# Kernel tuning notes

Measured on AMD Instinct MI355X. Metric: run time of the kernel, lower is better.

## Reference

```python
import jax, jax.numpy as jnp
import numpy as np

DIM = 768
HEADS = 12
HEAD_DIM = DIM // HEADS  # 64
B, T = 4, 2048


def setup_inputs() -> dict:
    key = jax.random.key(0)
    k1, k2, k3 = jax.random.split(key, 3)
    x = jax.random.normal(k1, (B, T, DIM), dtype=jnp.float32)
    w_qkv = jax.random.normal(k2, (DIM, 3 * DIM), dtype=jnp.float32) * (DIM ** -0.5)
    w_out = jax.random.normal(k3, (DIM, DIM), dtype=jnp.float32) * (DIM ** -0.5)
    b_out = jnp.zeros((DIM,), dtype=jnp.float32)
    return {"x": x, "w_qkv": w_qkv, "w_out": w_out, "b_out": b_out}


def reference(x, w_qkv, w_out, b_out):
    b, t, _ = x.shape
    # fused QKV projection (no bias)
    xp = x @ w_qkv                               # (b, t, 3*dim)
    # faithful to einops 'b t (d k h) -> k b h t d' with k=3, h=HEADS
    xp = xp.reshape(b, t, HEAD_DIM, 3, HEADS)
    qkv = jnp.transpose(xp, (3, 0, 4, 1, 2))     # (3, b, h, t, d)
    q, k, v = qkv[0], qkv[1], qkv[2]
    scores = jnp.einsum('bhid,bhjd->bhij', q, k) * (HEAD_DIM ** -0.5)
    attn = jax.nn.softmax(scores, axis=-1)
    out = jnp.einsum('bhij,bhjd->bhid', attn, v)  # (b, h, t, d)
    out = jnp.transpose(out, (0, 2, 1, 3)).reshape(b, t, HEADS * HEAD_DIM)
    return out @ w_out + b_out
```

## Files before the change

kernel.cpp:

```cpp
#include <hip/hip_runtime.h>
#include <hip/hip_bf16.h>


typedef short short8 __attribute__((ext_vector_type(8)));
typedef _Float16 half8 __attribute__((ext_vector_type(8)));
typedef _Float16 half2v __attribute__((ext_vector_type(2)));
typedef float f32x16 __attribute__((ext_vector_type(16)));
typedef unsigned int uint4v __attribute__((ext_vector_type(4)));
typedef unsigned short ushort8v __attribute__((ext_vector_type(8)));
typedef unsigned short ushort4v __attribute__((ext_vector_type(4)));
typedef unsigned short ushort;

__device__ __forceinline__ ushort f2h(float x) {
    _Float16 h = (_Float16)x;
    return __builtin_bit_cast(ushort, h);
}
__device__ __forceinline__ float h2f(ushort u) {
    return (float)__builtin_bit_cast(_Float16, u);
}
__device__ __forceinline__ unsigned pk2h(float lo, float hi) {
    return __builtin_bit_cast(unsigned, __builtin_amdgcn_cvt_pkrtz(lo, hi));
}
__device__ __forceinline__ float dot2acc(unsigned pair, float acc) {
    const half2v ones = {(_Float16)1.0f, (_Float16)1.0f};
    return __builtin_amdgcn_fdot2(__builtin_bit_cast(half2v, pair), ones, acc, false);
}
__device__ __forceinline__ short8 ldfrag(const ushort* buf, int row, int slotLogical) {
    int phys = slotLogical ^ (row & 7);
    return *reinterpret_cast<const short8*>(&buf[row * 64 + phys * 8]);
}
__device__ __forceinline__ f32x16 mfma16(half8 a, half8 b, f32x16 c) {
    return __builtin_amdgcn_mfma_f32_32x32x16_f16(a, b, c, 0, 0, 0);
}
__device__ __forceinline__ half8 ldfragh(const ushort* buf, int row, int slotLogical) {
    return __builtin_bit_cast(half8, ldfrag(buf, row, slotLogical));
}
__device__ __forceinline__ half8 ldh(const ushort* p) {
    return __builtin_bit_cast(half8, *reinterpret_cast<const short8*>(p));
}
__device__ __forceinline__ void gload16(const ushort* g, ushort* l) {
    __builtin_amdgcn_global_load_lds((__attribute__((address_space(1))) void*)g,
                                     (__attribute__((address_space(3))) void*)l, 16, 0, 0);
}

__global__ __launch_bounds__(256) void prep_all(const float* __restrict__ x,
                                                const float* __restrict__ wqkv,
                                                const float* __restrict__ wout,
                                                ushort* __restrict__ Xh,
                                                ushort* __restrict__ Wt,
                                                ushort* __restrict__ Wo) {
    int b = blockIdx.x;
    if (b < 3072) {
        long i8 = (long)(b * 256 + threadIdx.x) * 8;
        float4 v0 = *reinterpret_cast<const float4*>(&x[i8]);
        float4 v1 = *reinterpret_cast<const float4*>(&x[i8 + 4]);
        float v[8] = {v0.x, v0.y, v0.z, v0.w, v1.x, v1.y, v1.z, v1.w};
        ushort8v hh;
#pragma unroll
        for (int j = 0; j < 8; ++j) hh[j] = f2h(v[j]);
        *reinterpret_cast<ushort8v*>(&Xh[i8]) = hh;
    } else if (b < 3072 + 864) {
        int id = (b - 3072) * 256 + threadIdx.x;
        int n = id % 2304;
        int oct = id / 2304;
        int g = n >> 6, d = n & 63;
        int col = d * 36 + g;
        ushort8v hh;
#pragma unroll
        for (int i = 0; i < 8; ++i) hh[i] = f2h(wqkv[(long)(8 * oct + i) * 2304 + col]);
        *reinterpret_cast<ushort8v*>(&Wt[(long)n * 768 + 8 * oct]) = hh;
    } else {
        int id = (b - 3936) * 256 + threadIdx.x;
        int n = id % 768;
        int oct = id / 768;
        ushort8v hh;
#pragma unroll
        for (int i = 0; i < 8; ++i) hh[i] = f2h(wout[(long)(8 * oct + i) * 768 + n]);
        *reinterpret_cast<ushort8v*>(&Wo[(long)n * 768 + 8 * oct]) = hh;
    }
}

__device__ __forceinline__ void gemm_core(const ushort* __restrict__ A,
                                          const ushort* __restrict__ Bt,
                                          long aBase, long bBase,
                                          ushort* sA, ushort* sB, f32x16 (&acc)[2][2]) {
    const int tid = threadIdx.x;
    const int lane = tid & 63, w = tid >> 6;
    const int c31 = lane & 31, g1 = lane >> 5;
    const int wr = w >> 1, wc = w & 1;
    const int srow_in_chunk = lane >> 3;
    for (int k0 = 0; k0 < 768; k0 += 64) {
        __syncthreads();
#pragma unroll
        for (int t = 0; t < 4; ++t) {
            int row = w * 32 + t * 8 + srow_in_chunk;
            int sl = (lane & 7) ^ (row & 7);
            long goff = (long)row * 768 + k0 + sl * 8;
            int ldst = (w * 32 + t * 8) * 64;
            gload16(&A[aBase + goff], &sA[ldst]);
            gload16(&Bt[bBase + goff], &sB[ldst]);
        }
        __syncthreads();
#pragma unroll
        for (int ks = 0; ks < 4; ++ks) {
            half8 ah[2], bh[2];
#pragma unroll
            for (int i = 0; i < 2; ++i) {
                ah[i] = ldfragh(sA, wr * 64 + i * 32 + c31, 2 * ks + g1);
                bh[i] = ldfragh(sB, wc * 64 + i * 32 + c31, 2 * ks + g1);
            }
#pragma unroll
            for (int mi = 0; mi < 2; ++mi)
#pragma unroll
                for (int nj = 0; nj < 2; ++nj)
                    acc[mi][nj] = mfma16(ah[mi], bh[nj], acc[mi][nj]);
        }
    }
}

__global__ __launch_bounds__(256) void gemm_qkv(const ushort* __restrict__ Xh,
                                                const ushort* __restrict__ Wt,
                                                ushort* __restrict__ Qf,
                                                ushort* __restrict__ Kf,
                                                ushort* __restrict__ Vt) {
    __shared__ ushort sA[128 * 64];
    __shared__ ushort sB[128 * 64];
    const int by0 = blockIdx.y * 128, bx0 = blockIdx.x * 128;
    f32x16 acc[2][2] = {};
    gemm_core(Xh, Wt, (long)by0 * 768, (long)bx0 * 768, sA, sB, acc);

    const int tid = threadIdx.x, lane = tid & 63, w = tid >> 6;
    const int c31 = lane & 31, g1 = lane >> 5;
    const int wr = w >> 1, wc = w & 1;
    const int bb = by0 >> 11, tb = by0 & 2047;
#pragma unroll
    for (int nj = 0; nj < 2; ++nj) {
        int n = bx0 + wc * 64 + nj * 32 + c31;
        int gg = n >> 6;
        int d = n & 63;
        if (gg < 24) {
            int kq = gg >= 12;
            int hh = gg - kq * 12;
            ushort* Dst = kq ? Kf : Qf;
            float sc = kq ? 0.1803368801111204f : 1.0f;
            long cb = ((long)(bb * 12 + hh) * 2048) * 64 + d;
#pragma unroll
            for (int mi = 0; mi < 2; ++mi)
#pragma unroll
                for (int r = 0; r < 16; ++r) {
                    int t = tb + wr * 64 + mi * 32 + (r & 3) + 8 * (r >> 2) + 4 * g1;
                    Dst[cb + (long)t * 64] = f2h(acc[mi][nj][r] * sc);
                }
        } else {
            int hh = gg - 24;
            long vb = ((long)(bb * 12 + hh) * 64 + d) * 2048;
#pragma unroll
            for (int mi = 0; mi < 2; ++mi)
#pragma unroll
                for (int rq = 0; rq < 4; ++rq) {
                    int tq = tb + wr * 64 + mi * 32 + 8 * rq + 4 * g1;
                    ushort4v vv;
#pragma unroll
                    for (int j = 0; j < 4; ++j) vv[j] = f2h(acc[mi][nj][4 * rq + j]);
                    *reinterpret_cast<ushort4v*>(&Vt[vb + tq]) = vv;
                }
        }
    }
}

__global__ __launch_bounds__(256) void flash_attn(const ushort* __restrict__ Qf,
                                                  const ushort* __restrict__ Kf,
                                                  const ushort* __restrict__ Vt,
                                                  ushort* __restrict__ Op0,
                                                  ushort* __restrict__ Op1,
                                                  float* __restrict__ lp0,
                                                  float* __restrict__ lp1) {
    __shared__ ushort Ks[2][64 * 64];
    const int tid = threadIdx.x;
    const int w = tid >> 6;
    const int lane = tid & 63;
    const int c = lane & 31, g1 = lane >> 5;
    const int wgid = blockIdx.x;
    const int inner = (wgid >> 3) & 31;
    const int xblk = inner >> 1;
    const int kh = inner & 1;
    const int bh = (wgid & 7) + 8 * (wgid >> 8);
    const int t0 = xblk * 128 + w * 32;
    const long hb = (long)bh * 2048 * 64;
    const int jbase = kh * 1024;

    half8 qh[4];
    {
        const long qrow = hb + (long)(t0 + c) * 64;
#pragma unroll
        for (int ks = 0; ks < 4; ++ks)
            qh[ks] = ldh(&Qf[qrow + ks * 16 + g1 * 8]);
    }

    const int r0 = tid >> 3, sl = tid & 7, r1 = r0 + 32;
    const int off0 = r0 * 64 + ((sl ^ (r0 & 7)) * 8);
    const int off1 = r1 * 64 + ((sl ^ (r1 & 7)) * 8);

    {
        short8 a = *reinterpret_cast<const short8*>(&Kf[hb + (long)(jbase + r0) * 64 + sl * 8]);
        short8 b = *reinterpret_cast<const short8*>(&Kf[hb + (long)(jbase + r1) * 64 + sl * 8]);
        *reinterpret_cast<short8*>(&Ks[0][off0]) = a;
        *reinterpret_cast<short8*>(&Ks[0][off1]) = b;
    }
    const ushort* kst0 = &Kf[hb + (long)(jbase + 64 + r0) * 64 + sl * 8];
    const ushort* kst1 = &Kf[hb + (long)(jbase + 64 + r1) * 64 + sl * 8];
    const ushort* vp0 = &Vt[hb + (long)c * 2048 + jbase + g1 * 8];
    const ushort* vp1 = vp0 + 32 * 2048;
    __syncthreads();

    f32x16 o0 = {}, o1 = {};
    float lrun = 0.f;
    int cur = 0;

    for (int j = 0; j < 16; ++j) {
        half8 vf0[4], vf1[4];
        vf0[0] = ldh(vp0);      vf1[0] = ldh(vp1);
        vf0[1] = ldh(vp0 + 16); vf1[1] = ldh(vp1 + 16);

        f32x16 s0 = {}, s1 = {};
        __builtin_amdgcn_s_setprio(1);
#pragma unroll
        for (int ks = 0; ks < 4; ++ks) {
            int slot = 2 * ks + g1;
            half8 k0f = ldfragh(&Ks[cur][0], c, slot);
            half8 k1f = ldfragh(&Ks[cur][0], 32 + c, slot);
            s0 = mfma16(k0f, qh[ks], s0);
            s1 = mfma16(k1f, qh[ks], s1);
        }
        __builtin_amdgcn_s_setprio(0);

        vf0[2] = ldh(vp0 + 32); vf1[2] = ldh(vp1 + 32);
        vf0[3] = ldh(vp0 + 48); vf1[3] = ldh(vp1 + 48);
        vp0 += 64; vp1 += 64;

        short8 pk0, pk1;
        const bool nxt = j + 1 < 16;
        if (nxt) {
            pk0 = *reinterpret_cast<const short8*>(kst0);
            pk1 = *reinterpret_cast<const short8*>(kst1);
            kst0 += 4096; kst1 += 4096;
        }

#pragma unroll
        for (int r = 0; r < 16; ++r) {
            s0[r] = exp2f(s0[r]);
            s1[r] = exp2f(s1[r]);
        }

        __builtin_amdgcn_s_setprio(1);
#pragma unroll
        for (int ks = 0; ks < 4; ++ks) {
            const int b8 = (ks & 1) * 8;
            uint4v dv;
#pragma unroll
            for (int mi = 0; mi < 2; ++mi) {
                float aLo = (ks < 2) ? s0[2 * mi + b8] : s1[2 * mi + b8];
                float aHi = (ks < 2) ? s0[2 * mi + b8 + 1] : s1[2 * mi + b8 + 1];
                float bLo = (ks < 2) ? s0[2 * mi + b8 + 4] : s1[2 * mi + b8 + 4];
                float bHi = (ks < 2) ? s0[2 * mi + b8 + 5] : s1[2 * mi + b8 + 5];
                unsigned xA = pk2h(aLo, aHi);
                unsigned xB = pk2h(bLo, bHi);
                lrun = dot2acc(xA, lrun);
                lrun = dot2acc(xB, lrun);
                auto rr = __builtin_amdgcn_permlane32_swap(xA, xB, false, false);
                dv[mi] = rr[0];
                dv[2 + mi] = rr[1];
            }
            half8 pb = __builtin_bit_cast(half8, dv);
            o0 = mfma16(vf0[ks], pb, o0);
            o1 = mfma16(vf1[ks], pb, o1);
        }
        __builtin_amdgcn_s_setprio(0);

        if (nxt) {
            *reinterpret_cast<short8*>(&Ks[cur ^ 1][off0]) = pk0;
            *reinterpret_cast<short8*>(&Ks[cur ^ 1][off1]) = pk1;
        }
        __syncthreads();
        cur ^= 1;
    }

    const float ltot = lrun + __shfl_xor(lrun, 32);
    ushort* Op = kh ? Op1 : Op0;
    float* lp = kh ? lp1 : lp0;
    const long pbase = ((long)bh * 64) * 2048 + t0 + c;
#pragma unroll
    for (int r = 0; r < 16; ++r) {
        int d0 = (r & 3) + 8 * (r >> 2) + 4 * g1;
        Op[pbase + (long)d0 * 2048] = f2h(o0[r]);
        Op[pbase + (long)(32 + d0) * 2048] = f2h(o1[r]);
    }
    if (g1 == 0) lp[(long)bh * 2048 + t0 + c] = ltot;
}

__global__ __launch_bounds__(256) void combine(const ushort* __restrict__ Op0,
                                               const ushort* __restrict__ Op1,
                                               const float* __restrict__ lp0,
                                               const float* __restrict__ lp1,
                                               ushort* __restrict__ Of) {
    __shared__ float linv[64];
    __shared__ ushort tile[64][72];
    const int bh = blockIdx.x >> 5;
    const int tb = blockIdx.x & 31;
    const int t0 = tb * 64;
    const int tid = threadIdx.x;
    if (tid < 64)
        linv[tid] = 1.0f / (lp0[(long)bh * 2048 + t0 + tid] + lp1[(long)bh * 2048 + t0 + tid]);
    __syncthreads();
#pragma unroll
    for (int it = 0; it < 2; ++it) {
        int u = tid + 256 * it;
        int d = u & 63, tg = u >> 6;
        long base = ((long)bh * 64 + d) * 2048 + t0 + tg * 8;
        ushort8v a = *reinterpret_cast<const ushort8v*>(&Op0[base]);
        ushort8v b = *reinterpret_cast<const ushort8v*>(&Op1[base]);
#pragma unroll
        for (int j = 0; j < 8; ++j)
            tile[tg * 8 + j][d] = f2h((h2f(a[j]) + h2f(b[j])) * linv[tg * 8 + j]);
    }
    __syncthreads();
    const int bb = bh / 12, h = bh - bb * 12;
#pragma unroll
    for (int it = 0; it < 2; ++it) {
        int u = tid + 256 * it;
        int dg = u & 7, t = u >> 3;
        ushort8v v;
#pragma unroll
        for (int j = 0; j < 8; ++j) v[j] = tile[t][dg * 8 + j];
        *reinterpret_cast<ushort8v*>(&Of[((long)(bb * 2048) + t0 + t) * 768 + h * 64 + dg * 8]) = v;
    }
}

__global__ __launch_bounds__(256) void gemm_out(const ushort* __restrict__ Of,
                                                const ushort* __restrict__ Wo,
                                                const float* __restrict__ bias,
                                                float* __restrict__ Cout) {
    __shared__ ushort sA[128 * 64];
    __shared__ ushort sB[128 * 64];
    const int by0 = blockIdx.y * 128, bx0 = blockIdx.x * 128;
    f32x16 acc[2][2] = {};
    gemm_core(Of, Wo, (long)by0 * 768, (long)bx0 * 768, sA, sB, acc);

    const int tid = threadIdx.x, lane = tid & 63, w = tid >> 6;
    const int c31 = lane & 31, g1 = lane >> 5;
    const int wr = w >> 1, wc = w & 1;
#pragma unroll
    for (int nj = 0; nj < 2; ++nj) {
        int n = bx0 + wc * 64 + nj * 32 + c31;
        float bv = bias[n];
#pragma unroll
        for (int mi = 0; mi < 2; ++mi)
#pragma unroll
            for (int r = 0; r < 16; ++r) {
                int row = by0 + wr * 64 + mi * 32 + (r & 3) + 8 * (r >> 2) + 4 * g1;
                Cout[(long)row * 768 + n] = acc[mi][nj][r] + bv;
            }
    }
}

extern "C" void kernel_launch(void* const* d_in, const int* in_sizes, int n_in,
                              void* d_out, int out_size, void* d_ws, size_t ws_size,
                              hipStream_t stream) {
    const float* x     = (const float*)d_in[0];
    const float* w_qkv = (const float*)d_in[1];
    const float* w_out = (const float*)d_in[2];
    const float* b_out = (const float*)d_in[3];
    float* out = (float*)d_out;

    const long U = 12582912;
    char* p = (char*)d_ws;
    ushort* Xh  = (ushort*)(p);
    ushort* Wt  = (ushort*)(p + U);
    ushort* Wo  = (ushort*)(p + U + 3538944);
    ushort* Qf  = (ushort*)(p + U + 4718592);
    ushort* Kf  = Qf + 6291456;
    ushort* Vt  = Kf + 6291456;
    ushort* Op0 = Vt + 6291456;
    ushort* Op1 = Op0 + 6291456;
    float*  lp0 = (float*)(Op1 + 6291456);
    float*  lp1 = lp0 + 98304;
    ushort* Of  = Xh;

    prep_all  <<<4224, 256, 0, stream>>>(x, w_qkv, w_out, Xh, Wt, Wo);
    gemm_qkv  <<<dim3(18, 64), 256, 0, stream>>>(Xh, Wt, Qf, Kf, Vt);
    flash_attn<<<1536, 256, 0, stream>>>(Qf, Kf, Vt, Op0, Op1, lp0, lp1);
    combine   <<<1536, 256, 0, stream>>>(Op0, Op1, lp0, lp1, Of);
    gemm_out  <<<dim3(6, 64), 256, 0, stream>>>(Of, Wo, b_out, out);
}
```

Baseline: 209.2 us.

## Stage V tiles in LDS and software-pipeline QK^T one tile ahead

The flash attention loop now loads V tiles cooperatively into a double-buffered swizzled LDS array instead of each wave reading its V fragments straight from global memory. It also computes the next tile's QK^T scores before the current tile's exp and PV step, so matrix work overlaps the softmax arithmetic. K prefetch moves two tiles ahead. The cost is extra LDS (double-buffered K and V), more live registers for the second score accumulator, and extra LDS reads for V fragments, which may reduce occupancy.

```diff
diff --git a/kernel.cpp b/kernel.cpp
--- a/kernel.cpp
+++ b/kernel.cpp
@@ -34,9 +34,6 @@
 }
 __device__ __forceinline__ half8 ldfragh(const ushort* buf, int row, int slotLogical) {
     return __builtin_bit_cast(half8, ldfrag(buf, row, slotLogical));
-}
-__device__ __forceinline__ half8 ldh(const ushort* p) {
-    return __builtin_bit_cast(half8, *reinterpret_cast<const short8*>(p));
 }
 __device__ __forceinline__ void gload16(const ushort* g, ushort* l) {
     __builtin_amdgcn_global_load_lds((__attribute__((address_space(1))) void*)g,
@@ -176,6 +173,7 @@
                                                   float* __restrict__ lp0,
                                                   float* __restrict__ lp1) {
     __shared__ ushort Ks[2][64 * 64];
+    __shared__ ushort Vs[2][64 * 64];
     const int tid = threadIdx.x;
     const int w = tid >> 6;
     const int lane = tid & 63;
@@ -194,7 +192,7 @@
         const long qrow = hb + (long)(t0 + c) * 64;
 #pragma unroll
         for (int ks = 0; ks < 4; ++ks)
-            qh[ks] = ldh(&Qf[qrow + ks * 16 + g1 * 8]);
+            qh[ks] = __builtin_bit_cast(half8, *reinterpret_cast<const short8*>(&Qf[qrow + ks * 16 + g1 * 8]));
     }
 
     const int r0 = tid >> 3, sl = tid & 7, r1 = r0 + 32;
@@ -202,48 +200,68 @@
     const int off1 = r1 * 64 + ((sl ^ (r1 & 7)) * 8);
 
     {
-        short8 a = *reinterpret_cast<const short8*>(&Kf[hb + (long)(jbase + r0) * 64 + sl * 8]);
-        short8 b = *reinterpret_cast<const short8*>(&Kf[hb + (long)(jbase + r1) * 64 + sl * 8]);
-        *reinterpret_cast<short8*>(&Ks[0][off0]) = a;
-        *reinterpret_cast<short8*>(&Ks[0][off1]) = b;
-    }
-    const ushort* kst0 = &Kf[hb + (long)(jbase + 64 + r0) * 64 + sl * 8];
-    const ushort* kst1 = &Kf[hb + (long)(jbase + 64 + r1) * 64 + sl * 8];
-    const ushort* vp0 = &Vt[hb + (long)c * 2048 + jbase + g1 * 8];
-    const ushort* vp1 = vp0 + 32 * 2048;
+        short8 k00 = *reinterpret_cast<const short8*>(&Kf[hb + (long)(jbase + r0) * 64 + sl * 8]);
+        short8 k01 = *reinterpret_cast<const short8*>(&Kf[hb + (long)(jbase + r1) * 64 + sl * 8]);
+        short8 k10 = *reinterpret_cast<const short8*>(&Kf[hb + (long)(jbase + 64 + r0) * 64 + sl * 8]);
+        short8 k11 = *reinterpret_cast<const short8*>(&Kf[hb + (long)(jbase + 64 + r1) * 64 + sl * 8]);
+        short8 v00 = *reinterpret_cast<const short8*>(&Vt[hb + (long)r0 * 2048 + jbase + sl * 8]);
+        short8 v01 = *reinterpret_cast<const short8*>(&Vt[hb + (long)r1 * 2048 + jbase + sl * 8]);
+        *reinterpret_cast<short8*>(&Ks[0][off0]) = k00;
+        *reinterpret_cast<short8*>(&Ks[0][off1]) = k01;
+        *reinterpret_cast<short8*>(&Ks[1][off0]) = k10;
+        *reinterpret_cast<short8*>(&Ks[1][off1]) = k11;
+        *reinterpret_cast<short8*>(&Vs[0][off0]) = v00;
+        *reinterpret_cast<short8*>(&Vs[0][off1]) = v01;
+    }
     __syncthreads();
+
+    const ushort* kst0 = &Kf[hb + (long)(jbase + 128 + r0) * 64 + sl * 8];
+    const ushort* kst1 = &Kf[hb + (long)(jbase + 128 + r1) * 64 + sl * 8];
+    const ushort* vst0 = &Vt[hb + (long)r0 * 2048 + jbase + 64 + sl * 8];
+    const ushort* vst1 = &Vt[hb + (long)r1 * 2048 + jbase + 64 + sl * 8];
+
+    f32x16 s0 = {}, s1 = {};
+#pragma unroll
+    for (int ks = 0; ks < 4; ++ks) {
+        int slot = 2 * ks + g1;
+        half8 k0f = ldfragh(&Ks[0][0], c, slot);
+        half8 k1f = ldfragh(&Ks[0][0], 32 + c, slot);
+        s0 = mfma16(k0f, qh[ks], s0);
+        s1 = mfma16(k1f, qh[ks], s1);
+    }
 
     f32x16 o0 = {}, o1 = {};
     float lrun = 0.f;
-    int cur = 0;
 
     for (int j = 0; j < 16; ++j) {
-        half8 vf0[4], vf1[4];
-        vf0[0] = ldh(vp0);      vf1[0] = ldh(vp1);
-        vf0[1] = ldh(vp0 + 16); vf1[1] = ldh(vp1 + 16);
-
-        f32x16 s0 = {}, s1 = {};
-        __builtin_amdgcn_s_setprio(1);
-#pragma unroll
-        for (int ks = 0; ks < 4; ++ks) {
-            int slot = 2 * ks + g1;
-            half8 k0f = ldfragh(&Ks[cur][0], c, slot);
-            half8 k1f = ldfragh(&Ks[cur][0], 32 + c, slot);
-            s0 = mfma16(k0f, qh[ks], s0);
-            s1 = mfma16(k1f, qh[ks], s1);
-        }
-        __builtin_amdgcn_s_setprio(0);
-
-        vf0[2] = ldh(vp0 + 32); vf1[2] = ldh(vp1 + 32);
-        vf0[3] = ldh(vp0 + 48); vf1[3] = ldh(vp1 + 48);
-        vp0 += 64; vp1 += 64;
-
-        short8 pk0, pk1;
-        const bool nxt = j + 1 < 16;
-        if (nxt) {
+        const int par = j & 1;
+        const bool hasN1 = j + 1 < 16;
+        const bool hasN2 = j + 2 < 16;
+
+        f32x16 n0 = {}, n1 = {};
+        if (hasN1) {
+            __builtin_amdgcn_s_setprio(1);
+#pragma unroll
+            for (int ks = 0; ks < 4; ++ks) {
+                int slot = 2 * ks + g1;
+                half8 k0f = ldfragh(&Ks[par ^ 1][0], c, slot);
+                half8 k1f = ldfragh(&Ks[par ^ 1][0], 32 + c, slot);
+                n0 = mfma16(k0f, qh[ks], n0);
+                n1 = mfma16(k1f, qh[ks], n1);
+            }
+            __builtin_amdgcn_s_setprio(0);
+        }
+
+        short8 pk0, pk1, pv0, pv1;
+        if (hasN2) {
             pk0 = *reinterpret_cast<const short8*>(kst0);
             pk1 = *reinterpret_cast<const short8*>(kst1);
             kst0 += 4096; kst1 += 4096;
+        }
+        if (hasN1) {
+            pv0 = *reinterpret_cast<const short8*>(vst0);
+            pv1 = *reinterpret_cast<const short8*>(vst1);
+            vst0 += 64; vst1 += 64;
         }
 
 #pragma unroll
@@ -272,17 +290,25 @@
                 dv[2 + mi] = rr[1];
             }
             half8 pb = __builtin_bit_cast(half8, dv);
-            o0 = mfma16(vf0[ks], pb, o0);
-            o1 = mfma16(vf1[ks], pb, o1);
+            int slot = 2 * ks + g1;
+            half8 va0 = ldfragh(&Vs[par][0], c, slot);
+            half8 va1 = ldfragh(&Vs[par][0], 32 + c, slot);
+            o0 = mfma16(va0, pb, o0);
+            o1 = mfma16(va1, pb, o1);
         }
         __builtin_amdgcn_s_setprio(0);
 
-        if (nxt) {
-            *reinterpret_cast<short8*>(&Ks[cur ^ 1][off0]) = pk0;
-            *reinterpret_cast<short8*>(&Ks[cur ^ 1][off1]) = pk1;
+        if (hasN2) {
+            *reinterpret_cast<short8*>(&Ks[par][off0]) = pk0;
+            *reinterpret_cast<short8*>(&Ks[par][off1]) = pk1;
+        }
+        if (hasN1) {
+            *reinterpret_cast<short8*>(&Vs[par ^ 1][off0]) = pv0;
+            *reinterpret_cast<short8*>(&Vs[par ^ 1][off1]) = pv1;
         }
         __syncthreads();
-        cur ^= 1;
+
+        s0 = n0; s1 = n1;
     }
 
     const float ltot = lrun + __shfl_xor(lrun, 32);
```

Measured after the change: 191.0 us. -8.7%, faster.
